# Kernel tuning notes

Measured on AMD Instinct MI355X. Metric: run time of the kernel, lower is better.

## Reference

```python
import jax, jax.numpy as jnp
import numpy as np

EPS = 1e-12  # F.normalize default eps


def setup_inputs() -> dict:
    key = jax.random.key(0)
    k1, k2, k3, k4 = jax.random.split(key, 4)
    b, c, h, w = 4, 64, 256, 256
    n_class, n = 19, 20
    nc1 = n_class + 1
    content = jax.random.normal(k1, (b, c, h, w), dtype=jnp.float32)
    seg = jax.random.randint(k2, (b, h, w), 0, n_class, dtype=jnp.int32)
    # xavier-normal-ish init for memory params
    key_mem = jax.random.normal(k3, (nc1, c, n), dtype=jnp.float32) * np.sqrt(2.0 / (c + n))
    val_mem = jax.random.normal(k4, (nc1, n, c), dtype=jnp.float32) * np.sqrt(2.0 / (n + c))
    return {"content": content, "seg": seg, "key_mem": key_mem, "val_mem": val_mem}


def reference(content, seg, key_mem, val_mem):
    # content: [b,c,h,w]; seg: [b,h,w] int; key_mem: [K,c,n]; val_mem: [K,n,c], K=n_class+1
    b, c, h, w = content.shape
    K, _, n = key_mem.shape
    p = h * w
    # one-hot class routing (seg shifted by +1 as in original)
    onehot = jax.nn.one_hot(seg.reshape(b, p) + 1, K, dtype=content.dtype)  # [b,p,K]
    # L2-normalize content rows (masked rows in the original are either this
    # normalized vector, for the matching class, or exactly zero)
    cn = content.transpose(0, 2, 3, 1).reshape(b, p, c)
    cn = cn / jnp.maximum(jnp.linalg.norm(cn, axis=-1, keepdims=True), EPS)
    # L2-normalize keys over channel dim (dim=1 of [K,c,n])
    kn = key_mem / jnp.maximum(jnp.linalg.norm(key_mem, axis=1, keepdims=True), EPS)
    # scores for the matching class; non-matching rows are zero -> softmax = uniform 1/n
    scores = jnp.einsum('bpc,kcn->bkpn', cn, kn)         # [b,K,p,n]
    attn = jax.nn.softmax(scores, axis=-1)
    mask = onehot.transpose(0, 2, 1)[..., None]           # [b,K,p,1]
    weight = jnp.where(mask > 0, attn, 1.0 / n)           # [b,K,p,n]
    # bmm with values, then sum over class dim (fused into the einsum)
    out = jnp.einsum('bkpn,knc->bpc', weight, val_mem)    # [b,p,c]
    return out.reshape(b, h, w, c).transpose(0, 3, 1, 2)  # [b,c,h,w]
```

## Files before the change

kernel.cpp:

```cpp
#include <hip/hip_runtime.h>

typedef _Float16 h2 __attribute__((ext_vector_type(2)));
typedef _Float16 h8 __attribute__((ext_vector_type(8)));
typedef float f4 __attribute__((ext_vector_type(4)));
typedef unsigned int uint32;

#define NVAL 20
#define CDIM 64
#define HW   65536
#define NPIX (4*HW)

#define BLK   1024
#define NWAVE (BLK/64)
#define MAXTILES 35
#define MAXSLOT  (MAXTILES*64)

#define KN_OFF      0
#define KN_KSTRIDE  2560
#define VAL_OFF     (20*KN_KSTRIDE)
#define VAL_KSTRIDE 4096
#define VAL_CSTRIDE 64

#define ROW_STRIDE 144
#define ROWS_BYTES (BLK*ROW_STRIDE)
#define INV_OFF   ROWS_BYTES
#define PERM_OFF  (INV_OFF + BLK*4)
#define TCLS_OFF  (PERM_OFF + MAXSLOT*2)
#define FLAG_OFF  (TCLS_OFF + 144)
#define CNT_OFF   (FLAG_OFF + 144)
#define LDS_TOTAL (CNT_OFF + 24*4 + 16)

static __device__ __forceinline__ h2 bch2(uint32 u) { return __builtin_bit_cast(h2, u); }
static __device__ __forceinline__ uint32 bcu(h2 v) { return __builtin_bit_cast(uint32, v); }
static __device__ __forceinline__ h8 bch8(uint4 u) { return __builtin_bit_cast(h8, u); }
static __device__ __forceinline__ h2 pkrtz(float a, float b) {
    return __builtin_bit_cast(h2, __builtin_amdgcn_cvt_pkrtz(a, b));
}

__global__ void prep_kernel(const float* __restrict__ key,
                            const float* __restrict__ val,
                            unsigned char* __restrict__ ws) {
    int i = blockIdx.x * 256 + threadIdx.x;
    if (i < 20*CDIM) {
        int k = i >> 6, c = i & 63;
        const float* vb = val + k*NVAL*CDIM + c;
        float v[NVAL];
        float s = 0.f;
        #pragma unroll
        for (int j = 0; j < NVAL; j++) { v[j] = vb[j*CDIM]; s += v[j]; }
        float t = 0.f;
        for (int kk = 0; kk < 20; kk++) {
            const float* vb2 = val + kk*NVAL*CDIM + c;
            #pragma unroll
            for (int j = 0; j < NVAL; j++) t += vb2[j*CDIM];
        }
        float rest = (t - s) * (1.0f/NVAL);
        uint32* row = (uint32*)(ws + VAL_OFF + (size_t)k*VAL_KSTRIDE + c*VAL_CSTRIDE);
        #pragma unroll
        for (int jp = 0; jp < 10; jp++) row[jp] = bcu(pkrtz(v[2*jp], v[2*jp+1]));
        row[10] = bcu(pkrtz(rest, 0.f));
        #pragma unroll
        for (int jp = 11; jp < 16; jp++) row[jp] = 0u;
    } else if (i < 20*CDIM + 20*NVAL) {
        int idx = i - 20*CDIM;
        int k = idx / NVAL, j = idx % NVAL;
        const float* kb = key + k*CDIM*NVAL + j;
        float x[CDIM];
        float ssq = 0.f;
        #pragma unroll
        for (int c = 0; c < CDIM; c++) { x[c] = kb[c*NVAL]; ssq = fmaf(x[c], x[c], ssq); }
        float inv = 1.0f / fmaxf(sqrtf(ssq), 1e-12f);
        uint32* row = (uint32*)(ws + KN_OFF + (size_t)k*KN_KSTRIDE + j*128);
        #pragma unroll
        for (int cp = 0; cp < 32; cp++) row[cp] = bcu(pkrtz(x[2*cp]*inv, x[2*cp+1]*inv));
    }
}

static __device__ __forceinline__ int2 scan20(const int* cnt, int cls) {
    int acc = 0, mb = 0;
    #pragma unroll
    for (int k = 1; k <= 20; k++) {
        if (k == cls) mb = acc;
        acc += (cnt[k] + 63) & ~63;
    }
    return make_int2(mb, acc >> 6);
}

__global__ __launch_bounds__(BLK, 4) void main_kernel(
        const float* __restrict__ content, const int* __restrict__ seg,
        const unsigned char* __restrict__ tabs, float* __restrict__ out) {
    extern __shared__ unsigned char lds[];
    float* invA = (float*)(lds + INV_OFF);
    unsigned short* perm = (unsigned short*)(lds + PERM_OFF);
    int* tcls  = (int*)(lds + TCLS_OFF);
    int* flags = (int*)(lds + FLAG_OFF);
    int* cnt   = (int*)(lds + CNT_OFF);

    const int tid  = threadIdx.x;
    const int bid  = (int)((blockIdx.x & 7) * 32 + (blockIdx.x >> 3));
    const int gp0  = bid * BLK;
    const int b    = gp0 >> 16;
    const int pim0 = gp0 & (HW - 1);
    float* obase = out + (size_t)b * CDIM * HW + pim0;

    if (tid < 24) cnt[tid] = 0;
    if (tid < MAXTILES) flags[tid] = 0;
    for (int i = tid; i < MAXSLOT; i += BLK) perm[i] = 0xFFFFu;
    __syncthreads();

    const int cls = seg[gp0 + tid] + 1;
    const int myrank = atomicAdd(&cnt[cls], 1);

    {
        const float* cptr = content + (size_t)b * CDIM * HW + pim0 + tid;
        uint2* myrow = (uint2*)(lds + tid * ROW_STRIDE);
        float ssq = 0.f;
        #pragma unroll
        for (int q = 0; q < 16; q++) {
            float f0 = cptr[(size_t)(4*q+0) * HW];
            float f1 = cptr[(size_t)(4*q+1) * HW];
            float f2 = cptr[(size_t)(4*q+2) * HW];
            float f3 = cptr[(size_t)(4*q+3) * HW];
            ssq = fmaf(f0,f0,ssq); ssq = fmaf(f1,f1,ssq);
            ssq = fmaf(f2,f2,ssq); ssq = fmaf(f3,f3,ssq);
            uint2 o; o.x = bcu(pkrtz(f0,f1)); o.y = bcu(pkrtz(f2,f3));
            myrow[q] = o;
        }
        invA[tid] = 1.0f / fmaxf(sqrtf(ssq), 1e-12f);
    }
    __syncthreads();

    const int2 s = scan20(cnt, cls);
    const int myslot = s.x + myrank;
    const int mytile = myslot >> 6;
    {
        perm[myslot] = (unsigned short)tid;
        tcls[mytile] = cls;
    }
    __syncthreads();

    const int nt   = s.y;
    const int wave = tid >> 6, lane = tid & 63;
    const int g = lane >> 4, r16 = lane & 15;

    for (int t = wave; t < nt; t += NWAVE) {
        const int u = __builtin_amdgcn_readfirstlane(tcls[t]);

        int rowb[4];
        float invn[4];
        bool mine[4];
        #pragma unroll
        for (int n = 0; n < 4; n++) {
            int v = perm[t*64 + n*16 + r16];
            mine[n] = (v != 0xFFFF);
            int l = mine[n] ? v : 0;
            rowb[n] = l * ROW_STRIDE;
            invn[n] = invA[l];
        }

        const unsigned char* knc = tabs + KN_OFF + (size_t)u * KN_KSTRIDE;
        uint4 a_sc[2][2];
        #pragma unroll
        for (int m = 0; m < 2; m++)
            #pragma unroll
            for (int ks = 0; ks < 2; ks++)
                a_sc[m][ks] = *(const uint4*)(knc + (m*16 + r16)*128 + (ks*32 + g*8)*2);
        uint4 b_sc[4][2];
        #pragma unroll
        for (int n = 0; n < 4; n++)
            #pragma unroll
            for (int ks = 0; ks < 2; ks++)
                b_sc[n][ks] = *(const uint4*)(lds + rowb[n] + (ks*32 + g*8)*2);

        f4 sacc[2][4];
        #pragma unroll
        for (int m = 0; m < 2; m++)
            #pragma unroll
            for (int n = 0; n < 4; n++) sacc[m][n] = (f4){0.f,0.f,0.f,0.f};
        #pragma unroll
        for (int ks = 0; ks < 2; ks++)
            #pragma unroll
            for (int m = 0; m < 2; m++)
                #pragma unroll
                for (int n = 0; n < 4; n++)
                    sacc[m][n] = __builtin_amdgcn_mfma_f32_16x16x32_f16(
                        bch8(a_sc[m][ks]), bch8(b_sc[n][ks]), sacc[m][n], 0, 0, 0);

        uint2 w0[4], w1[4];
        #pragma unroll
        for (int n = 0; n < 4; n++) {
            float e0[4], e1[4];
            #pragma unroll
            for (int r = 0; r < 4; r++) e0[r] = __expf(sacc[0][n][r] * invn[n]);
            float arg1 = (g == 0) ? invn[n] : 0.0f;
            #pragma unroll
            for (int r = 0; r < 4; r++) e1[r] = __expf(sacc[1][n][r] * arg1);
            float sum = e0[0]+e0[1]+e0[2]+e0[3];
            sum += (g == 0) ? (e1[0]+e1[1]+e1[2]+e1[3]) : 0.0f;
            sum += __shfl_xor(sum, 16, 64);
            sum += __shfl_xor(sum, 32, 64);
            float wsc = 1.0f / sum;
            w0[n].x = bcu(pkrtz(e0[0]*wsc, e0[1]*wsc));
            w0[n].y = bcu(pkrtz(e0[2]*wsc, e0[3]*wsc));
            uint2 t1;
            if (g == 0)      { t1.x = bcu(pkrtz(e1[0]*wsc, e1[1]*wsc));
                               t1.y = bcu(pkrtz(e1[2]*wsc, e1[3]*wsc)); }
            else if (g == 1) { t1.x = 0x00003C00u; t1.y = 0u; }
            else             { t1.x = 0u; t1.y = 0u; }
            w1[n] = t1;
        }
        #pragma unroll
        for (int n = 0; n < 4; n++) {
            if (mine[n]) {
                *(uint2*)(lds + rowb[n] + g*8)      = w0[n];
                *(uint2*)(lds + rowb[n] + 32 + g*8) = w1[n];
            }
        }

        uint4 b_pv[4];
        #pragma unroll
        for (int n = 0; n < 4; n++)
            b_pv[n] = *(const uint4*)(lds + rowb[n] + g*16);
        const unsigned char* vc = tabs + VAL_OFF + (size_t)u * VAL_KSTRIDE;
        #pragma unroll
        for (int m = 0; m < 4; m++) {
            uint4 a = *(const uint4*)(vc + (m*16 + r16)*VAL_CSTRIDE + g*16);
            #pragma unroll
            for (int n = 0; n < 4; n++) {
                f4 o = (f4){0.f,0.f,0.f,0.f};
                o = __builtin_amdgcn_mfma_f32_16x16x32_f16(bch8(a), bch8(b_pv[n]), o, 0, 0, 0);
                uint2 ov; ov.x = bcu(pkrtz(o[0], o[1])); ov.y = bcu(pkrtz(o[2], o[3]));
                if (mine[n])
                    *(uint2*)(lds + rowb[n] + m*32 + g*8) = ov;
            }
        }

        __threadfence_block();
        if (lane == 0)
            __hip_atomic_store(&flags[t], 1, __ATOMIC_RELEASE, __HIP_MEMORY_SCOPE_WORKGROUP);
    }

    while (__hip_atomic_load(&flags[mytile], __ATOMIC_ACQUIRE,
                             __HIP_MEMORY_SCOPE_WORKGROUP) == 0) {
        __builtin_amdgcn_s_sleep(1);
    }
    {
        const uint4* r4 = (const uint4*)(lds + tid * ROW_STRIDE);
        float* op = obase + tid;
        #pragma unroll
        for (int q = 0; q < 8; q++) {
            uint4 v = r4[q];
            h2 x = bch2(v.x), y = bch2(v.y), z = bch2(v.z), w = bch2(v.w);
            op[(size_t)(8*q+0) * HW] = (float)x[0];
            op[(size_t)(8*q+1) * HW] = (float)x[1];
            op[(size_t)(8*q+2) * HW] = (float)y[0];
            op[(size_t)(8*q+3) * HW] = (float)y[1];
            op[(size_t)(8*q+4) * HW] = (float)z[0];
            op[(size_t)(8*q+5) * HW] = (float)z[1];
            op[(size_t)(8*q+6) * HW] = (float)w[0];
            op[(size_t)(8*q+7) * HW] = (float)w[1];
        }
    }
}

extern "C" void kernel_launch(void* const* d_in, const int* in_sizes, int n_in,
                              void* d_out, int out_size, void* d_ws, size_t ws_size,
                              hipStream_t stream) {
    const float* content = (const float*)d_in[0];
    const int*   seg     = (const int*)d_in[1];
    const float* key     = (const float*)d_in[2];
    const float* val     = (const float*)d_in[3];
    float* out = (float*)d_out;
    unsigned char* ws = (unsigned char*)d_ws;

    prep_kernel<<<7, 256, 0, stream>>>(key, val, ws);

    (void)hipFuncSetAttribute((const void*)main_kernel,
                              hipFuncAttributeMaxDynamicSharedMemorySize, LDS_TOTAL);
    main_kernel<<<NPIX/BLK, BLK, LDS_TOTAL, stream>>>(content, seg, ws, out);
}
```

Measured before the change: 40.85 us.

## Split content normalization into a separate kernel writing fp16 rows to workspace

Adds a norm_kernel that L2-normalizes every pixel's content vector and writes it as a contiguous fp16 row into workspace. The gather kernel then reads the B operands straight from global memory instead of staging them in LDS, and drops the per-pixel inverse-norm scaling in the softmax. This moves the strided channel loads and the normalization out of the LDS-heavy main kernel. The cost is an extra launch and a 32 MB intermediate round trip through HBM. The old fused kernel is kept as a fallback for when the workspace is too small.

```diff
diff --git a/kernel.cpp b/kernel.cpp
--- a/kernel.cpp
+++ b/kernel.cpp
@@ -20,15 +20,23 @@
 #define VAL_OFF     (20*KN_KSTRIDE)
 #define VAL_KSTRIDE 4096
 #define VAL_CSTRIDE 64
+#define XROWS_OFF   (VAL_OFF + 20*VAL_KSTRIDE)
+#define WS_NEED     (XROWS_OFF + (size_t)NPIX*128)
 
 #define ROW_STRIDE 144
 #define ROWS_BYTES (BLK*ROW_STRIDE)
-#define INV_OFF   ROWS_BYTES
-#define PERM_OFF  (INV_OFF + BLK*4)
+#define PERM_OFF  ROWS_BYTES
 #define TCLS_OFF  (PERM_OFF + MAXSLOT*2)
 #define FLAG_OFF  (TCLS_OFF + 144)
 #define CNT_OFF   (FLAG_OFF + 144)
 #define LDS_TOTAL (CNT_OFF + 24*4 + 16)
+
+#define FINV_OFF  ROWS_BYTES
+#define FPERM_OFF (FINV_OFF + BLK*4)
+#define FTCLS_OFF (FPERM_OFF + MAXSLOT*2)
+#define FFLAG_OFF (FTCLS_OFF + 144)
+#define FCNT_OFF  (FFLAG_OFF + 144)
+#define FLDS_TOTAL (FCNT_OFF + 24*4 + 16)
 
 static __device__ __forceinline__ h2 bch2(uint32 u) { return __builtin_bit_cast(h2, u); }
 static __device__ __forceinline__ uint32 bcu(h2 v) { return __builtin_bit_cast(uint32, v); }
@@ -86,11 +94,35 @@
     return make_int2(mb, acc >> 6);
 }
 
-__global__ __launch_bounds__(BLK, 4) void main_kernel(
-        const float* __restrict__ content, const int* __restrict__ seg,
-        const unsigned char* __restrict__ tabs, float* __restrict__ out) {
+__global__ __launch_bounds__(256) void norm_kernel(
+        const float* __restrict__ content, unsigned char* __restrict__ ws) {
+    const int gpix = blockIdx.x * 256 + threadIdx.x;
+    const int b = gpix >> 16, p = gpix & (HW - 1);
+    const float* cptr = content + (size_t)b * CDIM * HW + p;
+    float x[CDIM];
+    float ssq = 0.f;
+    #pragma unroll
+    for (int c = 0; c < CDIM; c++) {
+        x[c] = cptr[(size_t)c * HW];
+        ssq = fmaf(x[c], x[c], ssq);
+    }
+    const float inv = 1.0f / fmaxf(sqrtf(ssq), 1e-12f);
+    uint4* row = (uint4*)(ws + XROWS_OFF + (size_t)gpix * 128);
+    #pragma unroll
+    for (int q = 0; q < 8; q++) {
+        uint4 o;
+        o.x = bcu(pkrtz(x[8*q+0]*inv, x[8*q+1]*inv));
+        o.y = bcu(pkrtz(x[8*q+2]*inv, x[8*q+3]*inv));
+        o.z = bcu(pkrtz(x[8*q+4]*inv, x[8*q+5]*inv));
+        o.w = bcu(pkrtz(x[8*q+6]*inv, x[8*q+7]*inv));
+        row[q] = o;
+    }
+}
+
+__global__ __launch_bounds__(BLK, 4) void gather_kernel(
+        const int* __restrict__ seg, const unsigned char* __restrict__ tabs,
+        float* __restrict__ out) {
     extern __shared__ unsigned char lds[];
-    float* invA = (float*)(lds + INV_OFF);
     unsigned short* perm = (unsigned short*)(lds + PERM_OFF);
     int* tcls  = (int*)(lds + TCLS_OFF);
     int* flags = (int*)(lds + FLAG_OFF);
@@ -102,6 +134,7 @@
     const int b    = gp0 >> 16;
     const int pim0 = gp0 & (HW - 1);
     float* obase = out + (size_t)b * CDIM * HW + pim0;
+    const unsigned char* xrows = tabs + XROWS_OFF + (size_t)gp0 * 128;
 
     if (tid < 24) cnt[tid] = 0;
     if (tid < MAXTILES) flags[tid] = 0;
@@ -110,24 +143,6 @@
 
     const int cls = seg[gp0 + tid] + 1;
     const int myrank = atomicAdd(&cnt[cls], 1);
-
-    {
-        const float* cptr = content + (size_t)b * CDIM * HW + pim0 + tid;
-        uint2* myrow = (uint2*)(lds + tid * ROW_STRIDE);
-        float ssq = 0.f;
-        #pragma unroll
-        for (int q = 0; q < 16; q++) {
-            float f0 = cptr[(size_t)(4*q+0) * HW];
-            float f1 = cptr[(size_t)(4*q+1) * HW];
-            float f2 = cptr[(size_t)(4*q+2) * HW];
-            float f3 = cptr[(size_t)(4*q+3) * HW];
-            ssq = fmaf(f0,f0,ssq); ssq = fmaf(f1,f1,ssq);
-            ssq = fmaf(f2,f2,ssq); ssq = fmaf(f3,f3,ssq);
-            uint2 o; o.x = bcu(pkrtz(f0,f1)); o.y = bcu(pkrtz(f2,f3));
-            myrow[q] = o;
-        }
-        invA[tid] = 1.0f / fmaxf(sqrtf(ssq), 1e-12f);
-    }
     __syncthreads();
 
     const int2 s = scan20(cnt, cls);
@@ -147,15 +162,17 @@
         const int u = __builtin_amdgcn_readfirstlane(tcls[t]);
 
         int rowb[4];
-        float invn[4];
         bool mine[4];
+        uint4 b_sc[4][2];
         #pragma unroll
         for (int n = 0; n < 4; n++) {
             int v = perm[t*64 + n*16 + r16];
             mine[n] = (v != 0xFFFF);
             int l = mine[n] ? v : 0;
             rowb[n] = l * ROW_STRIDE;
-            invn[n] = invA[l];
+            const uint4* rp = (const uint4*)(xrows + (size_t)l * 128);
+            b_sc[n][0] = rp[g];
+            b_sc[n][1] = rp[4 + g];
         }
 
         const unsigned char* knc = tabs + KN_OFF + (size_t)u * KN_KSTRIDE;
@@ -165,12 +182,6 @@
             #pragma unroll
             for (int ks = 0; ks < 2; ks++)
                 a_sc[m][ks] = *(const uint4*)(knc + (m*16 + r16)*128 + (ks*32 + g*8)*2);
-        uint4 b_sc[4][2];
-        #pragma unroll
-        for (int n = 0; n < 4; n++)
-            #pragma unroll
-            for (int ks = 0; ks < 2; ks++)
-                b_sc[n][ks] = *(const uint4*)(lds + rowb[n] + (ks*32 + g*8)*2);
 
         f4 sacc[2][4];
         #pragma unroll
@@ -191,8 +202,8 @@
         for (int n = 0; n < 4; n++) {
             float e0[4], e1[4];
             #pragma unroll
-            for (int r = 0; r < 4; r++) e0[r] = __expf(sacc[0][n][r] * invn[n]);
-            float arg1 = (g == 0) ? invn[n] : 0.0f;
+            for (int r = 0; r < 4; r++) e0[r] = __expf(sacc[0][n][r]);
+            float arg1 = (g == 0) ? 1.0f : 0.0f;
             #pragma unroll
             for (int r = 0; r < 4; r++) e1[r] = __expf(sacc[1][n][r] * arg1);
             float sum = e0[0]+e0[1]+e0[2]+e0[3];
@@ -263,6 +274,173 @@
     }
 }
 
+__global__ __launch_bounds__(BLK, 4) void fb_kernel(
+        const float* __restrict__ content, const int* __restrict__ seg,
+        const unsigned char* __restrict__ tabs, float* __restrict__ out) {
+    extern __shared__ unsigned char lds[];
+    float* invA = (float*)(lds + FINV_OFF);
+    unsigned short* perm = (unsigned short*)(lds + FPERM_OFF);
+    int* tcls  = (int*)(lds + FTCLS_OFF);
+    int* flags = (int*)(lds + FFLAG_OFF);
+    int* cnt   = (int*)(lds + FCNT_OFF);
+
+    const int tid  = threadIdx.x;
+    const int bid  = (int)((blockIdx.x & 7) * 32 + (blockIdx.x >> 3));
+    const int gp0  = bid * BLK;
+    const int b    = gp0 >> 16;
+    const int pim0 = gp0 & (HW - 1);
+    float* obase = out + (size_t)b * CDIM * HW + pim0;
+
+    if (tid < 24) cnt[tid] = 0;
+    if (tid < MAXTILES) flags[tid] = 0;
+    for (int i = tid; i < MAXSLOT; i += BLK) perm[i] = 0xFFFFu;
+    __syncthreads();
+
+    const int cls = seg[gp0 + tid] + 1;
+    const int myrank = atomicAdd(&cnt[cls], 1);
+    {
+        const float* cptr = content + (size_t)b * CDIM * HW + pim0 + tid;
+        uint2* myrow = (uint2*)(lds + tid * ROW_STRIDE);
+        float ssq = 0.f;
+        #pragma unroll
+        for (int q = 0; q < 16; q++) {
+            float f0 = cptr[(size_t)(4*q+0) * HW];
+            float f1 = cptr[(size_t)(4*q+1) * HW];
+            float f2 = cptr[(size_t)(4*q+2) * HW];
+            float f3 = cptr[(size_t)(4*q+3) * HW];
+            ssq = fmaf(f0,f0,ssq); ssq = fmaf(f1,f1,ssq);
+            ssq = fmaf(f2,f2,ssq); ssq = fmaf(f3,f3,ssq);
+            uint2 o; o.x = bcu(pkrtz(f0,f1)); o.y = bcu(pkrtz(f2,f3));
+            myrow[q] = o;
+        }
+        invA[tid] = 1.0f / fmaxf(sqrtf(ssq), 1e-12f);
+    }
+    __syncthreads();
+
+    const int2 s = scan20(cnt, cls);
+    const int myslot = s.x + myrank;
+    const int mytile = myslot >> 6;
+    perm[myslot] = (unsigned short)tid;
+    tcls[mytile] = cls;
+    __syncthreads();
+
+    const int nt   = s.y;
+    const int wave = tid >> 6, lane = tid & 63;
+    const int g = lane >> 4, r16 = lane & 15;
+
+    for (int t = wave; t < nt; t += NWAVE) {
+        const int u = __builtin_amdgcn_readfirstlane(tcls[t]);
+        int rowb[4];
+        float invn[4];
+        bool mine[4];
+        #pragma unroll
+        for (int n = 0; n < 4; n++) {
+            int v = perm[t*64 + n*16 + r16];
+            mine[n] = (v != 0xFFFF);
+            int l = mine[n] ? v : 0;
+            rowb[n] = l * ROW_STRIDE;
+            invn[n] = invA[l];
+        }
+        const unsigned char* knc = tabs + KN_OFF + (size_t)u * KN_KSTRIDE;
+        uint4 a_sc[2][2];
+        #pragma unroll
+        for (int m = 0; m < 2; m++)
+            #pragma unroll
+            for (int ks = 0; ks < 2; ks++)
+                a_sc[m][ks] = *(const uint4*)(knc + (m*16 + r16)*128 + (ks*32 + g*8)*2);
+        uint4 b_sc[4][2];
+        #pragma unroll
+        for (int n = 0; n < 4; n++)
+            #pragma unroll
+            for (int ks = 0; ks < 2; ks++)
+                b_sc[n][ks] = *(const uint4*)(lds + rowb[n] + (ks*32 + g*8)*2);
+        f4 sacc[2][4];
+        #pragma unroll
+        for (int m = 0; m < 2; m++)
+            #pragma unroll
+            for (int n = 0; n < 4; n++) sacc[m][n] = (f4){0.f,0.f,0.f,0.f};
+        #pragma unroll
+        for (int ks = 0; ks < 2; ks++)
+            #pragma unroll
+            for (int m = 0; m < 2; m++)
+                #pragma unroll
+                for (int n = 0; n < 4; n++)
+                    sacc[m][n] = __builtin_amdgcn_mfma_f32_16x16x32_f16(
+                        bch8(a_sc[m][ks]), bch8(b_sc[n][ks]), sacc[m][n], 0, 0, 0);
+        uint2 w0[4], w1[4];
+        #pragma unroll
+        for (int n = 0; n < 4; n++) {
+            float e0[4], e1[4];
+            #pragma unroll
+            for (int r = 0; r < 4; r++) e0[r] = __expf(sacc[0][n][r] * invn[n]);
+            float arg1 = (g == 0) ? invn[n] : 0.0f;
+            #pragma unroll
+            for (int r = 0; r < 4; r++) e1[r] = __expf(sacc[1][n][r] * arg1);
+            float sum = e0[0]+e0[1]+e0[2]+e0[3];
+            sum += (g == 0) ? (e1[0]+e1[1]+e1[2]+e1[3]) : 0.0f;
+            sum += __shfl_xor(sum, 16, 64);
+            sum += __shfl_xor(sum, 32, 64);
+            float wsc = 1.0f / sum;
+            w0[n].x = bcu(pkrtz(e0[0]*wsc, e0[1]*wsc));
+            w0[n].y = bcu(pkrtz(e0[2]*wsc, e0[3]*wsc));
+            uint2 t1;
+            if (g == 0)      { t1.x = bcu(pkrtz(e1[0]*wsc, e1[1]*wsc));
+                               t1.y = bcu(pkrtz(e1[2]*wsc, e1[3]*wsc)); }
+            else if (g == 1) { t1.x = 0x00003C00u; t1.y = 0u; }
+            else             { t1.x = 0u; t1.y = 0u; }
+            w1[n] = t1;
+        }
+        #pragma unroll
+        for (int n = 0; n < 4; n++) {
+            if (mine[n]) {
+                *(uint2*)(lds + rowb[n] + g*8)      = w0[n];
+                *(uint2*)(lds + rowb[n] + 32 + g*8) = w1[n];
+            }
+        }
+        uint4 b_pv[4];
+        #pragma unroll
+        for (int n = 0; n < 4; n++)
+            b_pv[n] = *(const uint4*)(lds + rowb[n] + g*16);
+        const unsigned char* vc = tabs + VAL_OFF + (size_t)u * VAL_KSTRIDE;
+        #pragma unroll
+        for (int m = 0; m < 4; m++) {
+            uint4 a = *(const uint4*)(vc + (m*16 + r16)*VAL_CSTRIDE + g*16);
+            #pragma unroll
+            for (int n = 0; n < 4; n++) {
+                f4 o = (f4){0.f,0.f,0.f,0.f};
+                o = __builtin_amdgcn_mfma_f32_16x16x32_f16(bch8(a), bch8(b_pv[n]), o, 0, 0, 0);
+                uint2 ov; ov.x = bcu(pkrtz(o[0], o[1])); ov.y = bcu(pkrtz(o[2], o[3]));
+                if (mine[n])
+                    *(uint2*)(lds + rowb[n] + m*32 + g*8) = ov;
+            }
+        }
+        __threadfence_block();
+        if (lane == 0)
+            __hip_atomic_store(&flags[t], 1, __ATOMIC_RELEASE, __HIP_MEMORY_SCOPE_WORKGROUP);
+    }
+    while (__hip_atomic_load(&flags[mytile], __ATOMIC_ACQUIRE,
+                             __HIP_MEMORY_SCOPE_WORKGROUP) == 0) {
+        __builtin_amdgcn_s_sleep(1);
+    }
+    {
+        const uint4* r4 = (const uint4*)(lds + tid * ROW_STRIDE);
+        float* op = obase + tid;
+        #pragma unroll
+        for (int q = 0; q < 8; q++) {
+            uint4 v = r4[q];
+            h2 x = bch2(v.x), y = bch2(v.y), z = bch2(v.z), w = bch2(v.w);
+            op[(size_t)(8*q+0) * HW] = (float)x[0];
+            op[(size_t)(8*q+1) * HW] = (float)x[1];
+            op[(size_t)(8*q+2) * HW] = (float)y[0];
+            op[(size_t)(8*q+3) * HW] = (float)y[1];
+            op[(size_t)(8*q+4) * HW] = (float)z[0];
+            op[(size_t)(8*q+5) * HW] = (float)z[1];
+            op[(size_t)(8*q+6) * HW] = (float)w[0];
+            op[(size_t)(8*q+7) * HW] = (float)w[1];
+        }
+    }
+}
+
 extern "C" void kernel_launch(void* const* d_in, const int* in_sizes, int n_in,
                               void* d_out, int out_size, void* d_ws, size_t ws_size,
                               hipStream_t stream) {
@@ -275,7 +453,14 @@
 
     prep_kernel<<<7, 256, 0, stream>>>(key, val, ws);
 
-    (void)hipFuncSetAttribute((const void*)main_kernel,
-                              hipFuncAttributeMaxDynamicSharedMemorySize, LDS_TOTAL);
-    main_kernel<<<NPIX/BLK, BLK, LDS_TOTAL, stream>>>(content, seg, ws, out);
-}
+    if (ws_size >= WS_NEED) {
+        norm_kernel<<<NPIX/256, 256, 0, stream>>>(content, ws);
+        (void)hipFuncSetAttribute((const void*)gather_kernel,
+                                  hipFuncAttributeMaxDynamicSharedMemorySize, LDS_TOTAL);
+        gather_kernel<<<NPIX/BLK, BLK, LDS_TOTAL, stream>>>(seg, ws, out);
+    } else {
+        (void)hipFuncSetAttribute((const void*)fb_kernel,
+                                  hipFuncAttributeMaxDynamicSharedMemorySize, FLDS_TOTAL);
+        fb_kernel<<<NPIX/BLK, BLK, FLDS_TOTAL, stream>>>(content, seg, ws, out);
+    }
+}
```

Result: slower. 57.57 us (+40.9%).

## Replace block-wide class sort with per-wave masked class loop

Applied to the files above, without the earlier changes.

Drops the per-block counting sort of pixels by class, along with its atomics, permutation tables, block barriers and spin-wait flags. Each wave now processes its own 64 pixels directly, looping over the classes present and masking the MFMA B operands by class so each pixel accumulates only its own class's scores and values. Blocks shrink from 1024 to 256 threads and use static LDS, and normalization is folded into the fp16 row before the MFMAs. The cost is redundant MFMA work per class present in a wave, which with random segmentation is most of the 19 classes.

```diff
diff --git a/kernel.cpp b/kernel.cpp
--- a/kernel.cpp
+++ b/kernel.cpp
@@ -10,10 +10,7 @@
 #define HW   65536
 #define NPIX (4*HW)
 
-#define BLK   1024
-#define NWAVE (BLK/64)
-#define MAXTILES 35
-#define MAXSLOT  (MAXTILES*64)
+#define BLK 256
 
 #define KN_OFF      0
 #define KN_KSTRIDE  2560
@@ -22,19 +19,22 @@
 #define VAL_CSTRIDE 64
 
 #define ROW_STRIDE 144
-#define ROWS_BYTES (BLK*ROW_STRIDE)
-#define INV_OFF   ROWS_BYTES
-#define PERM_OFF  (INV_OFF + BLK*4)
-#define TCLS_OFF  (PERM_OFF + MAXSLOT*2)
-#define FLAG_OFF  (TCLS_OFF + 144)
-#define CNT_OFF   (FLAG_OFF + 144)
-#define LDS_TOTAL (CNT_OFF + 24*4 + 16)
 
 static __device__ __forceinline__ h2 bch2(uint32 u) { return __builtin_bit_cast(h2, u); }
 static __device__ __forceinline__ uint32 bcu(h2 v) { return __builtin_bit_cast(uint32, v); }
 static __device__ __forceinline__ h8 bch8(uint4 u) { return __builtin_bit_cast(h8, u); }
 static __device__ __forceinline__ h2 pkrtz(float a, float b) {
     return __builtin_bit_cast(h2, __builtin_amdgcn_cvt_pkrtz(a, b));
+}
+static __device__ __forceinline__ uint4 sel4(bool p, uint4 v) {
+    uint4 r;
+    r.x = p ? v.x : 0u; r.y = p ? v.y : 0u;
+    r.z = p ? v.z : 0u; r.w = p ? v.w : 0u;
+    return r;
+}
+static __device__ __forceinline__ void wavefence() {
+    asm volatile("s_waitcnt lgkmcnt(0)" ::: "memory");
+    __builtin_amdgcn_wave_barrier();
 }
 
 __global__ void prep_kernel(const float* __restrict__ key,
@@ -76,177 +76,182 @@
     }
 }
 
-static __device__ __forceinline__ int2 scan20(const int* cnt, int cls) {
-    int acc = 0, mb = 0;
-    #pragma unroll
-    for (int k = 1; k <= 20; k++) {
-        if (k == cls) mb = acc;
-        acc += (cnt[k] + 63) & ~63;
-    }
-    return make_int2(mb, acc >> 6);
-}
-
 __global__ __launch_bounds__(BLK, 4) void main_kernel(
         const float* __restrict__ content, const int* __restrict__ seg,
         const unsigned char* __restrict__ tabs, float* __restrict__ out) {
-    extern __shared__ unsigned char lds[];
-    float* invA = (float*)(lds + INV_OFF);
-    unsigned short* perm = (unsigned short*)(lds + PERM_OFF);
-    int* tcls  = (int*)(lds + TCLS_OFF);
-    int* flags = (int*)(lds + FLAG_OFF);
-    int* cnt   = (int*)(lds + CNT_OFF);
+    __shared__ unsigned char lds[BLK * ROW_STRIDE];
 
     const int tid  = threadIdx.x;
-    const int bid  = (int)((blockIdx.x & 7) * 32 + (blockIdx.x >> 3));
-    const int gp0  = bid * BLK;
-    const int b    = gp0 >> 16;
-    const int pim0 = gp0 & (HW - 1);
-    float* obase = out + (size_t)b * CDIM * HW + pim0;
-
-    if (tid < 24) cnt[tid] = 0;
-    if (tid < MAXTILES) flags[tid] = 0;
-    for (int i = tid; i < MAXSLOT; i += BLK) perm[i] = 0xFFFFu;
-    __syncthreads();
-
-    const int cls = seg[gp0 + tid] + 1;
-    const int myrank = atomicAdd(&cnt[cls], 1);
-
-    {
-        const float* cptr = content + (size_t)b * CDIM * HW + pim0 + tid;
-        uint2* myrow = (uint2*)(lds + tid * ROW_STRIDE);
-        float ssq = 0.f;
-        #pragma unroll
-        for (int q = 0; q < 16; q++) {
-            float f0 = cptr[(size_t)(4*q+0) * HW];
-            float f1 = cptr[(size_t)(4*q+1) * HW];
-            float f2 = cptr[(size_t)(4*q+2) * HW];
-            float f3 = cptr[(size_t)(4*q+3) * HW];
-            ssq = fmaf(f0,f0,ssq); ssq = fmaf(f1,f1,ssq);
-            ssq = fmaf(f2,f2,ssq); ssq = fmaf(f3,f3,ssq);
-            uint2 o; o.x = bcu(pkrtz(f0,f1)); o.y = bcu(pkrtz(f2,f3));
-            myrow[q] = o;
-        }
-        invA[tid] = 1.0f / fmaxf(sqrtf(ssq), 1e-12f);
-    }
-    __syncthreads();
-
-    const int2 s = scan20(cnt, cls);
-    const int myslot = s.x + myrank;
-    const int mytile = myslot >> 6;
-    {
-        perm[myslot] = (unsigned short)tid;
-        tcls[mytile] = cls;
-    }
-    __syncthreads();
-
-    const int nt   = s.y;
     const int wave = tid >> 6, lane = tid & 63;
     const int g = lane >> 4, r16 = lane & 15;
-
-    for (int t = wave; t < nt; t += NWAVE) {
-        const int u = __builtin_amdgcn_readfirstlane(tcls[t]);
-
-        int rowb[4];
-        float invn[4];
-        bool mine[4];
-        #pragma unroll
-        for (int n = 0; n < 4; n++) {
-            int v = perm[t*64 + n*16 + r16];
-            mine[n] = (v != 0xFFFF);
-            int l = mine[n] ? v : 0;
-            rowb[n] = l * ROW_STRIDE;
-            invn[n] = invA[l];
-        }
-
-        const unsigned char* knc = tabs + KN_OFF + (size_t)u * KN_KSTRIDE;
-        uint4 a_sc[2][2];
+    const int bid = (int)((blockIdx.x & 7) * 128 + (blockIdx.x >> 3));
+    const int gp0 = bid * BLK;
+    const int b   = gp0 >> 16;
+    const int pix = (gp0 & (HW - 1)) + tid;
+    const float* cptr = content + (size_t)b * CDIM * HW + pix;
+
+    {
+        float xa[32], xc[32];
+        #pragma unroll
+        for (int j = 0; j < 32; j++) xa[j] = cptr[(size_t)j * HW];
+        #pragma unroll
+        for (int j = 0; j < 32; j++) xc[j] = cptr[(size_t)(32 + j) * HW];
+        float ssq = 0.f;
+        #pragma unroll
+        for (int j = 0; j < 32; j++) ssq = fmaf(xa[j], xa[j], ssq);
+        #pragma unroll
+        for (int j = 0; j < 32; j++) ssq = fmaf(xc[j], xc[j], ssq);
+        const float inv = 1.0f / fmaxf(sqrtf(ssq), 1e-12f);
+        uint4* myrow = (uint4*)(lds + tid * ROW_STRIDE);
+        #pragma unroll
+        for (int q = 0; q < 4; q++) {
+            uint4 o;
+            o.x = bcu(pkrtz(xa[8*q+0]*inv, xa[8*q+1]*inv));
+            o.y = bcu(pkrtz(xa[8*q+2]*inv, xa[8*q+3]*inv));
+            o.z = bcu(pkrtz(xa[8*q+4]*inv, xa[8*q+5]*inv));
+            o.w = bcu(pkrtz(xa[8*q+6]*inv, xa[8*q+7]*inv));
+            myrow[q] = o;
+        }
+        #pragma unroll
+        for (int q = 0; q < 4; q++) {
+            uint4 o;
+            o.x = bcu(pkrtz(xc[8*q+0]*inv, xc[8*q+1]*inv));
+            o.y = bcu(pkrtz(xc[8*q+2]*inv, xc[8*q+3]*inv));
+            o.z = bcu(pkrtz(xc[8*q+4]*inv, xc[8*q+5]*inv));
+            o.w = bcu(pkrtz(xc[8*q+6]*inv, xc[8*q+7]*inv));
+            myrow[q + 4] = o;
+        }
+    }
+    const int mycls = seg[gp0 + tid] + 1;
+
+    wavefence();
+
+    int clsv[4];
+    int rowb[4];
+    #pragma unroll
+    for (int n = 0; n < 4; n++) {
+        clsv[n] = __shfl(mycls, n*16 + r16, 64);
+        rowb[n] = (wave*64 + n*16 + r16) * ROW_STRIDE;
+    }
+
+    uint4 b_sc[4][2];
+    #pragma unroll
+    for (int n = 0; n < 4; n++)
+        #pragma unroll
+        for (int ks = 0; ks < 2; ks++)
+            b_sc[n][ks] = *(const uint4*)(lds + rowb[n] + ks*64 + g*16);
+
+    f4 sacc[2][4];
+    #pragma unroll
+    for (int m = 0; m < 2; m++)
+        #pragma unroll
+        for (int n = 0; n < 4; n++) sacc[m][n] = (f4){0.f,0.f,0.f,0.f};
+
+    #pragma unroll 1
+    for (int k = 1; k < 20; ++k) {
+        bool an[4];
+        #pragma unroll
+        for (int n = 0; n < 4; n++) an[n] = __any(clsv[n] == k);
+        if (!(an[0] | an[1] | an[2] | an[3])) continue;
+        const unsigned char* knc = tabs + KN_OFF + (size_t)k * KN_KSTRIDE;
+        uint4 ak[2][2];
         #pragma unroll
         for (int m = 0; m < 2; m++)
             #pragma unroll
             for (int ks = 0; ks < 2; ks++)
-                a_sc[m][ks] = *(const uint4*)(knc + (m*16 + r16)*128 + (ks*32 + g*8)*2);
-        uint4 b_sc[4][2];
-        #pragma unroll
-        for (int n = 0; n < 4; n++)
+                ak[m][ks] = *(const uint4*)(knc + (m*16 + r16)*128 + ks*64 + g*16);
+        #pragma unroll
+        for (int n = 0; n < 4; n++) {
+            if (!an[n]) continue;
+            const bool p = (clsv[n] == k);
+            uint4 mb0 = sel4(p, b_sc[n][0]);
+            uint4 mb1 = sel4(p, b_sc[n][1]);
+            sacc[0][n] = __builtin_amdgcn_mfma_f32_16x16x32_f16(bch8(ak[0][0]), bch8(mb0), sacc[0][n], 0, 0, 0);
+            sacc[0][n] = __builtin_amdgcn_mfma_f32_16x16x32_f16(bch8(ak[0][1]), bch8(mb1), sacc[0][n], 0, 0, 0);
+            sacc[1][n] = __builtin_amdgcn_mfma_f32_16x16x32_f16(bch8(ak[1][0]), bch8(mb0), sacc[1][n], 0, 0, 0);
+            sacc[1][n] = __builtin_amdgcn_mfma_f32_16x16x32_f16(bch8(ak[1][1]), bch8(mb1), sacc[1][n], 0, 0, 0);
+        }
+    }
+
+    uint2 w0[4], w1[4];
+    #pragma unroll
+    for (int n = 0; n < 4; n++) {
+        float e0[4], e1[4];
+        #pragma unroll
+        for (int r = 0; r < 4; r++) e0[r] = __expf(sacc[0][n][r]);
+        const float arg1 = (g == 0) ? 1.0f : 0.0f;
+        #pragma unroll
+        for (int r = 0; r < 4; r++) e1[r] = __expf(sacc[1][n][r] * arg1);
+        float sum = e0[0]+e0[1]+e0[2]+e0[3];
+        sum += (g == 0) ? (e1[0]+e1[1]+e1[2]+e1[3]) : 0.0f;
+        sum += __shfl_xor(sum, 16, 64);
+        sum += __shfl_xor(sum, 32, 64);
+        const float wsc = 1.0f / sum;
+        w0[n].x = bcu(pkrtz(e0[0]*wsc, e0[1]*wsc));
+        w0[n].y = bcu(pkrtz(e0[2]*wsc, e0[3]*wsc));
+        uint2 t1;
+        if (g == 0)      { t1.x = bcu(pkrtz(e1[0]*wsc, e1[1]*wsc));
+                           t1.y = bcu(pkrtz(e1[2]*wsc, e1[3]*wsc)); }
+        else if (g == 1) { t1.x = 0x00003C00u; t1.y = 0u; }
+        else             { t1.x = 0u; t1.y = 0u; }
+        w1[n] = t1;
+    }
+    #pragma unroll
+    for (int n = 0; n < 4; n++) {
+        *(uint2*)(lds + rowb[n] + g*8)      = w0[n];
+        *(uint2*)(lds + rowb[n] + 32 + g*8) = w1[n];
+    }
+
+    wavefence();
+
+    uint4 b_pv[4];
+    #pragma unroll
+    for (int n = 0; n < 4; n++)
+        b_pv[n] = *(const uint4*)(lds + rowb[n] + g*16);
+
+    f4 o[4][4];
+    #pragma unroll
+    for (int m = 0; m < 4; m++)
+        #pragma unroll
+        for (int n = 0; n < 4; n++) o[m][n] = (f4){0.f,0.f,0.f,0.f};
+
+    #pragma unroll 1
+    for (int k = 1; k < 20; ++k) {
+        bool an[4];
+        #pragma unroll
+        for (int n = 0; n < 4; n++) an[n] = __any(clsv[n] == k);
+        if (!(an[0] | an[1] | an[2] | an[3])) continue;
+        const unsigned char* vc = tabs + VAL_OFF + (size_t)k * VAL_KSTRIDE;
+        uint4 av[4];
+        #pragma unroll
+        for (int m = 0; m < 4; m++)
+            av[m] = *(const uint4*)(vc + (m*16 + r16)*VAL_CSTRIDE + g*16);
+        #pragma unroll
+        for (int n = 0; n < 4; n++) {
+            if (!an[n]) continue;
+            const bool p = (clsv[n] == k);
+            uint4 mbv = sel4(p, b_pv[n]);
             #pragma unroll
-            for (int ks = 0; ks < 2; ks++)
-                b_sc[n][ks] = *(const uint4*)(lds + rowb[n] + (ks*32 + g*8)*2);
-
-        f4 sacc[2][4];
-        #pragma unroll
-        for (int m = 0; m < 2; m++)
-            #pragma unroll
-            for (int n = 0; n < 4; n++) sacc[m][n] = (f4){0.f,0.f,0.f,0.f};
-        #pragma unroll
-        for (int ks = 0; ks < 2; ks++)
-            #pragma unroll
-            for (int m = 0; m < 2; m++)
-                #pragma unroll
-                for (int n = 0; n < 4; n++)
-                    sacc[m][n] = __builtin_amdgcn_mfma_f32_16x16x32_f16(
-                        bch8(a_sc[m][ks]), bch8(b_sc[n][ks]), sacc[m][n], 0, 0, 0);
-
-        uint2 w0[4], w1[4];
+            for (int m = 0; m < 4; m++)
+                o[m][n] = __builtin_amdgcn_mfma_f32_16x16x32_f16(bch8(av[m]), bch8(mbv), o[m][n], 0, 0, 0);
+        }
+    }
+
+    #pragma unroll
+    for (int m = 0; m < 4; m++)
         #pragma unroll
         for (int n = 0; n < 4; n++) {
-            float e0[4], e1[4];
-            #pragma unroll
-            for (int r = 0; r < 4; r++) e0[r] = __expf(sacc[0][n][r] * invn[n]);
-            float arg1 = (g == 0) ? invn[n] : 0.0f;
-            #pragma unroll
-            for (int r = 0; r < 4; r++) e1[r] = __expf(sacc[1][n][r] * arg1);
-            float sum = e0[0]+e0[1]+e0[2]+e0[3];
-            sum += (g == 0) ? (e1[0]+e1[1]+e1[2]+e1[3]) : 0.0f;
-            sum += __shfl_xor(sum, 16, 64);
-            sum += __shfl_xor(sum, 32, 64);
-            float wsc = 1.0f / sum;
-            w0[n].x = bcu(pkrtz(e0[0]*wsc, e0[1]*wsc));
-            w0[n].y = bcu(pkrtz(e0[2]*wsc, e0[3]*wsc));
-            uint2 t1;
-            if (g == 0)      { t1.x = bcu(pkrtz(e1[0]*wsc, e1[1]*wsc));
-                               t1.y = bcu(pkrtz(e1[2]*wsc, e1[3]*wsc)); }
-            else if (g == 1) { t1.x = 0x00003C00u; t1.y = 0u; }
-            else             { t1.x = 0u; t1.y = 0u; }
-            w1[n] = t1;
-        }
-        #pragma unroll
-        for (int n = 0; n < 4; n++) {
-            if (mine[n]) {
-                *(uint2*)(lds + rowb[n] + g*8)      = w0[n];
-                *(uint2*)(lds + rowb[n] + 32 + g*8) = w1[n];
-            }
-        }
-
-        uint4 b_pv[4];
-        #pragma unroll
-        for (int n = 0; n < 4; n++)
-            b_pv[n] = *(const uint4*)(lds + rowb[n] + g*16);
-        const unsigned char* vc = tabs + VAL_OFF + (size_t)u * VAL_KSTRIDE;
-        #pragma unroll
-        for (int m = 0; m < 4; m++) {
-            uint4 a = *(const uint4*)(vc + (m*16 + r16)*VAL_CSTRIDE + g*16);
-            #pragma unroll
-            for (int n = 0; n < 4; n++) {
-                f4 o = (f4){0.f,0.f,0.f,0.f};
-                o = __builtin_amdgcn_mfma_f32_16x16x32_f16(bch8(a), bch8(b_pv[n]), o, 0, 0, 0);
-                uint2 ov; ov.x = bcu(pkrtz(o[0], o[1])); ov.y = bcu(pkrtz(o[2], o[3]));
-                if (mine[n])
-                    *(uint2*)(lds + rowb[n] + m*32 + g*8) = ov;
-            }
-        }
-
-        __threadfence_block();
-        if (lane == 0)
-            __hip_atomic_store(&flags[t], 1, __ATOMIC_RELEASE, __HIP_MEMORY_SCOPE_WORKGROUP);
-    }
-
-    while (__hip_atomic_load(&flags[mytile], __ATOMIC_ACQUIRE,
-                             __HIP_MEMORY_SCOPE_WORKGROUP) == 0) {
-        __builtin_amdgcn_s_sleep(1);
-    }
+            uint2 ov;
+            ov.x = bcu(pkrtz(o[m][n][0], o[m][n][1]));
+            ov.y = bcu(pkrtz(o[m][n][2], o[m][n][3]));
+            *(uint2*)(lds + rowb[n] + m*32 + g*8) = ov;
+        }
+
+    wavefence();
+
     {
         const uint4* r4 = (const uint4*)(lds + tid * ROW_STRIDE);
-        float* op = obase + tid;
+        float* op = out + (size_t)b * CDIM * HW + pix;
         #pragma unroll
         for (int q = 0; q < 8; q++) {
             uint4 v = r4[q];
@@ -274,8 +279,5 @@
     unsigned char* ws = (unsigned char*)d_ws;
 
     prep_kernel<<<7, 256, 0, stream>>>(key, val, ws);
-
-    (void)hipFuncSetAttribute((const void*)main_kernel,
-                              hipFuncAttributeMaxDynamicSharedMemorySize, LDS_TOTAL);
-    main_kernel<<<NPIX/BLK, BLK, LDS_TOTAL, stream>>>(content, seg, ws, out);
-}
+    main_kernel<<<NPIX/BLK, BLK, 0, stream>>>(content, seg, ws, out);
+}
```

After: 78.74 us. +92.7%, slower.
